# Optimization experiments

Measured on AMD Instinct MI355X. Metric: run time of the kernel, lower is better.

## Reference

```python
import jax, jax.numpy as jnp
import numpy as np

PERIOD = 0.1


def setup_inputs() -> dict:
    key = jax.random.key(0)
    ks = jax.random.split(key, 16)
    B, N, C, P = 2, 3072, 4, 4
    E, H, T, F, L = 512, 8, 256, 64, 4
    Nt = N // P

    def rn(k, shape, scale=0.02):
        return jax.random.normal(k, shape, jnp.float32) * scale

    return {
        "x": jax.random.normal(ks[0], (B, N, C), jnp.float32),
        "t": jax.random.normal(ks[1], (B, T), jnp.float32),
        "vec_map": jax.random.normal(ks[2], (B, N, 3), jnp.float32),
        # RelativeBias dense: freq features -> heads
        "W_rb": rn(ks[3], (F, H)),
        "b_rb": jnp.zeros((H,), jnp.float32),
        # patch embedding dense: P*C -> E
        "W_embed": rn(ks[4], (P * C, E), 0.1),
        "b_embed": jnp.zeros((E,), jnp.float32),
        "pos_emb": rn(ks[5], (Nt, E)),
        # stacked per-block params (leading dim L = n_blocks)
        "ada1_W1": rn(ks[6], (L, T, T)),
        "ada1_b1": jnp.zeros((L, T), jnp.float32),
        "ada1_W2": rn(ks[7], (L, T, 3 * E)),
        "ada1_b2": jnp.zeros((L, 3 * E), jnp.float32),
        "qkv_W": rn(ks[8], (L, E, 3 * E)),
        "qkv_b": jnp.zeros((L, 3 * E), jnp.float32),
        "out_W": rn(ks[9], (L, E, E)),
        "out_b": jnp.zeros((L, E), jnp.float32),
        "ada2_W1": rn(ks[10], (L, T, T)),
        "ada2_b1": jnp.zeros((L, T), jnp.float32),
        "ada2_W2": rn(ks[11], (L, T, 3 * E)),
        "ada2_b2": jnp.zeros((L, 3 * E), jnp.float32),
        "mlp_W1": rn(ks[12], (L, E, 4 * E)),
        "mlp_b1": jnp.zeros((L, 4 * E), jnp.float32),
        "mlp_W2": rn(ks[13], (L, 4 * E, E)),
        "mlp_b2": jnp.zeros((L, E), jnp.float32),
    }


def _layernorm(y):
    # flax LayerNorm(use_bias=False, use_scale=False), eps=1e-6
    mu = jnp.mean(y, axis=-1, keepdims=True)
    var = jnp.mean(jnp.square(y - mu), axis=-1, keepdims=True)
    return (y - mu) * jax.lax.rsqrt(var + 1e-6)


def _adaln(t, W1, b1, W2, b2):
    h = jax.nn.silu(t @ W1 + b1)
    m = (h @ W2 + b2)[..., None, :]  # (B, 1, 3E)
    return jnp.split(m, 3, axis=-1)


def reference(x, t, vec_map, W_rb, b_rb, W_embed, b_embed, pos_emb,
              ada1_W1, ada1_b1, ada1_W2, ada1_b2, qkv_W, qkv_b, out_W, out_b,
              ada2_W1, ada2_b1, ada2_W2, ada2_b2, mlp_W1, mlp_b1, mlp_W2, mlp_b2):
    B, N, C = x.shape
    Nt, E = pos_emb.shape
    P = N // Nt
    F, H = W_rb.shape
    hd = E // H

    # patchify tokens: (B, N, C) -> (B, Nt, P*C); mean vec per patch
    xp = x.reshape(B, Nt, P * C)
    vp = vec_map.reshape(B, Nt, P, 3).mean(axis=-2)

    # relative bias logits (B, Nt, Nt, H)
    v = vp / jnp.linalg.norm(vp, axis=-1, keepdims=True)
    dif = v[..., :, None, :] - v[..., None, :, :]
    dot = 1.0 - 0.5 * jnp.sum(dif * dif, axis=-1)
    angle = jnp.arccos(jnp.clip(dot, -1.0, 1.0)) / 0.005
    freqs = jnp.linspace(0, 1, F // 2) / PERIOD
    ph = freqs * angle[..., None]  # (B, Nt, Nt, F/2)
    pos = jnp.concatenate((jnp.sin(ph), jnp.cos(ph)), axis=-1)
    bias = pos @ W_rb + b_rb

    # patch embed + learned positional embedding
    h0 = xp @ W_embed + b_embed + pos_emb
    inv_sqrt_hd = 1.0 / jnp.sqrt(jnp.float32(hd))

    def block(xc, params):
        (aW1, ab1, aW2, ab2, qW, qb, oW, ob,
         cW1, cb1, cW2, cb2, mW1, mb1, mW2, mb2) = params
        g1, be1, al1 = _adaln(t, aW1, ab1, aW2, ab2)
        y = (g1 + 1.0) * _layernorm(xc) + be1
        qkv = (y @ qW + qb).reshape(B, Nt, H, 3, hd)
        q, k, vv = qkv[..., 0, :], qkv[..., 1, :], qkv[..., 2, :]
        logits = jnp.einsum('bqht,bkht->bqkh', q, k) * inv_sqrt_hd + bias
        logits = logits - jnp.max(logits, axis=-2, keepdims=True)
        attn = jax.nn.softmax(logits, axis=-2)  # softmax over keys (K axis)
        y = jnp.einsum('bqkh,bkht->bqht', attn, vv).reshape(B, Nt, E)
        y = y @ oW + ob
        xc = xc + al1 * y / jnp.sqrt(1.0 + al1 * al1)
        g2, be2, al2 = _adaln(t, cW1, cb1, cW2, cb2)
        y = (g2 + 1.0) * _layernorm(xc) + be2
        y = jax.nn.gelu(y @ mW1 + mb1) @ mW2 + mb2
        xc = xc + al2 * y / jnp.sqrt(1.0 + al2 * al2)
        return xc, None

    params = (ada1_W1, ada1_b1, ada1_W2, ada1_b2, qkv_W, qkv_b, out_W, out_b,
              ada2_W1, ada2_b1, ada2_W2, ada2_b2, mlp_W1, mlp_b1, mlp_W2, mlp_b2)
    out, _ = jax.lax.scan(block, h0, params)
    return out
```

## Files before the change

### kernel.cpp

```cpp
#include <hip/hip_runtime.h>
#include <hip/hip_bf16.h>


#define NT 768
#define EDIM 512
#define E3 1536
#define E4 2048
#define NH 8
#define TB 2

typedef unsigned short ushort_t;
typedef __attribute__((ext_vector_type(8))) short bf16x8;
typedef __attribute__((ext_vector_type(4))) float f32x4;

#define GLOAD(src, dst) __builtin_amdgcn_global_load_lds( \
    (const __attribute__((address_space(1))) unsigned int*)(src), \
    (__attribute__((address_space(3))) unsigned int*)(dst), 16, 0, 0)

__device__ inline float b2f(ushort_t u) {
    unsigned int i = ((unsigned int)u) << 16; float f;
    __builtin_memcpy(&f, &i, 4); return f;
}
__device__ inline ushort_t f2b(float f) {
    __hip_bfloat16 h = __float2bfloat16(f);
    ushort_t u; __builtin_memcpy(&u, &h, 2); return u;
}
__device__ inline float gelu_tanh(float u) {
    float z = 1.5957691216057308f * (u + 0.044715f * u * u * u);
    z = fminf(z, 40.f);
    float t = __expf(z);
    float th = (t - 1.f) / (t + 1.f);
    return 0.5f * u * (1.f + th);
}

__global__ __launch_bounds__(256) void k_bias(const float* __restrict__ vm, const float* __restrict__ W_rb,
                                              const float* __restrict__ b_rb, ushort_t* __restrict__ biasT) {
    int bq = blockIdx.x; int b = bq / NT, q = bq % NT;
    __shared__ float sv[NT * 3];
    int tid = threadIdx.x, lane = tid & 63, wave = tid >> 6;
    for (int i = tid; i < NT; i += 256) {
        const float* vp = vm + ((long)b * 3072 + i * 4) * 3;
        float s0 = vp[0] + vp[3] + vp[6] + vp[9];
        float s1 = vp[1] + vp[4] + vp[7] + vp[10];
        float s2 = vp[2] + vp[5] + vp[8] + vp[11];
        float inv = rsqrtf(s0 * s0 + s1 * s1 + s2 * s2);
        sv[i * 3 + 0] = s0 * inv; sv[i * 3 + 1] = s1 * inv; sv[i * 3 + 2] = s2 * inv;
    }

    int g = lane >> 4, col = lane & 15;
    ushort_t tw[16];
    #pragma unroll
    for (int j = 0; j < 8; ++j) {
        float wsv = (col < 8) ? W_rb[(g * 8 + j) * 8 + col] : 0.f;
        float wcv = (col < 8) ? W_rb[(32 + g * 8 + j) * 8 + col] : 0.f;
        tw[j] = f2b(wsv); tw[8 + j] = f2b(wcv);
    }
    bf16x8 bsf, bcf;
    __builtin_memcpy(&bsf, tw, 16);
    __builtin_memcpy(&bcf, tw + 8, 16);
    float brh = (col < 8) ? b_rb[col] : 0.f;
    __syncthreads();

    float vq0 = sv[q * 3], vq1 = sv[q * 3 + 1], vq2 = sv[q * 3 + 2];
    float gf = (float)(8 * g);

    for (int it = 0; it < 12; ++it) {
        int tile = (it * 4 + wave) * 16;
        int p = tile + col;
        float d0 = vq0 - sv[p * 3], d1 = vq1 - sv[p * 3 + 1], d2 = vq2 - sv[p * 3 + 2];
        float dot = 1.f - 0.5f * (d0 * d0 + d1 * d1 + d2 * d2);
        dot = fminf(1.f, fmaxf(-1.f, dot));
        float theta = acosf(dot) * (2000.f / 31.f);
        float s1, c1; __sincosf(theta, &s1, &c1);
        float sg, cg; __sincosf(theta * gf, &sg, &cg);
        ushort_t fs[16];
        #pragma unroll
        for (int j = 0; j < 8; ++j) {
            fs[j] = f2b(sg); fs[8 + j] = f2b(cg);
            float ns = sg * c1 + cg * s1;
            cg = cg * c1 - sg * s1;
            sg = ns;
        }
        bf16x8 asf, acf;
        __builtin_memcpy(&asf, fs, 16);
        __builtin_memcpy(&acf, fs + 8, 16);
        f32x4 acc = {0.f, 0.f, 0.f, 0.f};
        acc = __builtin_amdgcn_mfma_f32_16x16x32_bf16(asf, bsf, acc, 0, 0, 0);
        acc = __builtin_amdgcn_mfma_f32_16x16x32_bf16(acf, bcf, acc, 0, 0, 0);
        if (col < 8) {
            ushort_t o[4];
            #pragma unroll
            for (int r = 0; r < 4; ++r) o[r] = f2b(acc[r] + brh);
            long off = (long)(b * 8 + col) * NT * NT + (long)q * NT + tile + 4 * g;
            uint2 pk;
            pk.x = (unsigned int)o[0] | ((unsigned int)o[1] << 16);
            pk.y = (unsigned int)o[2] | ((unsigned int)o[3] << 16);
            *(uint2*)(biasT + off) = pk;
        }
    }
}

__global__ __launch_bounds__(256) void k_embed(const float* __restrict__ x, const float* __restrict__ W,
                                               const float* __restrict__ be, const float* __restrict__ pe,
                                               float* __restrict__ xc) {
    int row = blockIdx.x; int nt = row % NT;
    __shared__ float sx[16];
    int tid = threadIdx.x;
    if (tid < 16) sx[tid] = x[row * 16 + tid];
    __syncthreads();
    for (int e = tid; e < EDIM; e += 256) {
        float a = be[e] + pe[nt * EDIM + e];
        #pragma unroll
        for (int j = 0; j < 16; ++j) a += sx[j] * W[j * EDIM + e];
        xc[(long)row * EDIM + e] = a;
    }
}

__global__ __launch_bounds__(256) void k_adaln(const float* __restrict__ t,
    const float* __restrict__ a1W1, const float* __restrict__ a1b1, const float* __restrict__ a1W2, const float* __restrict__ a1b2,
    const float* __restrict__ a2W1, const float* __restrict__ a2b1, const float* __restrict__ a2W2, const float* __restrict__ a2b2,
    float* __restrict__ ada) {
    int blk = blockIdx.x; int b = blk & 1, lw = blk >> 1; int which = lw & 1, l = lw >> 1;
    const float* W1 = (which ? a2W1 : a1W1) + (long)l * 256 * 256;
    const float* b1 = (which ? a2b1 : a1b1) + l * 256;
    const float* W2 = (which ? a2W2 : a1W2) + (long)l * 256 * E3;
    const float* b2 = (which ? a2b2 : a1b2) + l * E3;
    __shared__ float st[256], sh[256];
    int tid = threadIdx.x;
    st[tid] = t[b * 256 + tid];
    __syncthreads();
    float a = b1[tid];
    for (int i = 0; i < 256; ++i) a += st[i] * W1[i * 256 + tid];
    sh[tid] = a / (1.f + __expf(-a));
    __syncthreads();
    int c = blockIdx.y * 256 + tid;
    float m = b2[c];
    for (int i = 0; i < 256; ++i) m += sh[i] * W2[i * E3 + c];
    ada[(long)(lw * 2 + b) * E3 + c] = m;
}

__global__ __launch_bounds__(256) void k_lnmod(const float* __restrict__ xc, const float* __restrict__ ada,
                                               ushort_t* __restrict__ out, int lw) {
    int row = blockIdx.x; int b = row / NT;
    const float* ap = ada + (long)(lw * 2 + b) * E3;
    int tid = threadIdx.x;
    float2 vv = *(const float2*)(xc + (long)row * EDIM + tid * 2);
    float s1 = vv.x + vv.y, s2 = vv.x * vv.x + vv.y * vv.y;
    for (int o = 32; o; o >>= 1) { s1 += __shfl_down(s1, o); s2 += __shfl_down(s2, o); }
    __shared__ float sr[8];
    if ((tid & 63) == 0) { sr[tid >> 6] = s1; sr[4 + (tid >> 6)] = s2; }
    __syncthreads();
    s1 = sr[0] + sr[1] + sr[2] + sr[3];
    s2 = sr[4] + sr[5] + sr[6] + sr[7];
    float mu = s1 * (1.f / 512.f);
    float var = s2 * (1.f / 512.f) - mu * mu;
    float inv = rsqrtf(var + 1e-6f);
    int e = tid * 2;
    float r0 = (ap[e] + 1.f) * ((vv.x - mu) * inv) + ap[512 + e];
    float r1 = (ap[e + 1] + 1.f) * ((vv.y - mu) * inv) + ap[512 + e + 1];
    unsigned int pk = (unsigned int)f2b(r0) | ((unsigned int)f2b(r1) << 16);
    ((unsigned int*)out)[(long)row * 256 + tid] = pk;
}

__global__ __launch_bounds__(256) void k_wTall(
        const float* __restrict__ qkvW, const float* __restrict__ outW,
        const float* __restrict__ m1W, const float* __restrict__ m2W,
        ushort_t* __restrict__ qkvWt, ushort_t* __restrict__ outWt,
        ushort_t* __restrict__ m1Wt, ushort_t* __restrict__ m2Wt) {
    int idx = blockIdx.x, l = blockIdx.y;
    const float* W; ushort_t* Wt; int Kd, Nd, ntile, ktile;
    if (idx < 192)      { W = qkvW; Wt = qkvWt; Kd = 512;  Nd = 1536; ntile = idx % 24; ktile = idx / 24; }
    else if (idx < 256) { W = outW; Wt = outWt; Kd = 512;  Nd = 512;  idx -= 192; ntile = idx % 8;  ktile = idx / 8; }
    else if (idx < 512) { W = m1W;  Wt = m1Wt;  Kd = 512;  Nd = 2048; idx -= 256; ntile = idx % 32; ktile = idx / 32; }
    else                { W = m2W;  Wt = m2Wt;  Kd = 2048; Nd = 512;  idx -= 512; ntile = idx % 8;  ktile = idx / 8; }
    const float* Wp = W + (long)l * Kd * Nd;
    ushort_t* Wtp = Wt + (long)l * Kd * Nd;
    int n0 = ntile * 64, k0 = ktile * 64;
    __shared__ float s[64][65];
    int tid = threadIdx.x;
    #pragma unroll
    for (int it = 0; it < 4; ++it) {
        int i2 = tid + it * 256;
        int r = i2 >> 4, c4 = (i2 & 15) * 4;
        float4 vv = *(const float4*)(Wp + (long)(k0 + r) * Nd + n0 + c4);
        s[r][c4] = vv.x; s[r][c4 + 1] = vv.y; s[r][c4 + 2] = vv.z; s[r][c4 + 3] = vv.w;
    }
    __syncthreads();
    #pragma unroll
    for (int it = 0; it < 4; ++it) {
        int i2 = tid + it * 256;
        int rn = i2 >> 4, ck = (i2 & 15) * 4;
        long base = (long)(n0 + rn) * Kd + k0 + ck;
        #pragma unroll
        for (int j = 0; j < 4; ++j) Wtp[base + j] = f2b(s[ck + j][rn]);
    }
}

__global__ __launch_bounds__(256) void k_attn(const ushort_t* __restrict__ qkv16,
        const ushort_t* __restrict__ vT, const ushort_t* __restrict__ biasT,
        ushort_t* __restrict__ attnb) {
    int qt = blockIdx.x, bh = blockIdx.y;
    int b = bh >> 3, h = bh & 7;
    __shared__ __align__(16) ushort_t Ks[2][4096];
    __shared__ __align__(16) ushort_t Vs[2][4096];
    __shared__ __align__(16) ushort_t Bi[2][4096];
    int tid = threadIdx.x, lane = tid & 63, wave = tid >> 6;
    int g = lane >> 4, c = lane & 15;
    int ls = lane & 7, lr = lane >> 3;
    int stg_col = (ls ^ lr) * 8;
    int q0 = qt * 64;

    bf16x8 aq[2];
    {
        const ushort_t* qp = qkv16 + ((long)(b * NT + q0 + wave * 16 + c) * E3) + h * 192;
        aq[0] = *(const bf16x8*)(qp + g * 8);
        aq[1] = *(const bf16x8*)(qp + 32 + g * 8);
    }
    float m_r[4], l_r[4];
    f32x4 o_acc[4];
    #pragma unroll
    for (int rr = 0; rr < 4; ++rr) { m_r[rr] = -1e30f; l_r[rr] = 0.f; }
    #pragma unroll
    for (int nf = 0; nf < 4; ++nf) o_acc[nf] = f32x4{0.f, 0.f, 0.f, 0.f};

#define STAGEA(buf, kt) { \
        int k0_ = (kt) * 64; \
        _Pragma("unroll") \
        for (int is = 0; is < 2; ++is) { \
            int row = is * 32 + wave * 8 + lr; \
            int dstb = (is * 32 + wave * 8) * 64; \
            GLOAD(qkv16 + (long)(b * NT + k0_ + row) * E3 + h * 192 + 64 + stg_col, &Ks[buf][dstb]); \
            GLOAD(vT + ((long)bh * 64 + row) * NT + k0_ + stg_col, &Vs[buf][dstb]); \
            GLOAD(biasT + (long)bh * NT * NT + (long)(q0 + row) * NT + k0_ + ls * 8, &Bi[buf][dstb]); \
        } }

    STAGEA(0, 0);
    __syncthreads();
    int cur = 0;
    for (int kt = 0; kt < 12; ++kt) {
        if (kt + 1 < 12) STAGEA(cur ^ 1, kt + 1);
        f32x4 s[4];
        #pragma unroll
        for (int nf = 0; nf < 4; ++nf) {
            s[nf] = f32x4{0.f, 0.f, 0.f, 0.f};
            #pragma unroll
            for (int kh = 0; kh < 2; ++kh) {
                int row = nf * 16 + c;
                bf16x8 bk = *(const bf16x8*)(&Ks[cur][row * 64 + (((kh * 4 + g) ^ (row & 7))) * 8]);
                s[nf] = __builtin_amdgcn_mfma_f32_16x16x32_bf16(aq[kh], bk, s[nf], 0, 0, 0);
            }
        }
        float p[4][4], mt[4];
        #pragma unroll
        for (int rr = 0; rr < 4; ++rr) {
            int ql = wave * 16 + g * 4 + rr;
            #pragma unroll
            for (int nf = 0; nf < 4; ++nf)
                p[nf][rr] = s[nf][rr] * 0.125f + b2f(Bi[cur][ql * 64 + nf * 16 + c]);
            float mx = fmaxf(fmaxf(p[0][rr], p[1][rr]), fmaxf(p[2][rr], p[3][rr]));
            mx = fmaxf(mx, __shfl_xor(mx, 1));
            mx = fmaxf(mx, __shfl_xor(mx, 2));
            mx = fmaxf(mx, __shfl_xor(mx, 4));
            mx = fmaxf(mx, __shfl_xor(mx, 8));
            mt[rr] = mx;
        }
        #pragma unroll
        for (int rr = 0; rr < 4; ++rr) {
            float mnew = fmaxf(m_r[rr], mt[rr]);
            float sc = __expf(m_r[rr] - mnew);
            m_r[rr] = mnew;
            float rsum = 0.f;
            #pragma unroll
            for (int nf = 0; nf < 4; ++nf) {
                p[nf][rr] = __expf(p[nf][rr] - mnew);
                rsum += p[nf][rr];
            }
            rsum += __shfl_xor(rsum, 1); rsum += __shfl_xor(rsum, 2);
            rsum += __shfl_xor(rsum, 4); rsum += __shfl_xor(rsum, 8);
            l_r[rr] = l_r[rr] * sc + rsum;
            #pragma unroll
            for (int nf = 0; nf < 4; ++nf) o_acc[nf][rr] *= sc;
        }
        #pragma unroll
        for (int nf = 0; nf < 4; ++nf) {
            int kl = nf * 16 + c;
            int slot = kl >> 3, win = kl & 7;
            #pragma unroll
            for (int rr = 0; rr < 4; ++rr) {
                int ql = wave * 16 + g * 4 + rr;
                Bi[cur][ql * 64 + ((slot ^ (ql & 7)) * 8) + win] = f2b(p[nf][rr]);
            }
        }
        asm volatile("s_waitcnt lgkmcnt(0)" ::: "memory");
        bf16x8 ap[2];
        #pragma unroll
        for (int kh = 0; kh < 2; ++kh) {
            int ql = wave * 16 + c;
            ap[kh] = *(const bf16x8*)(&Bi[cur][ql * 64 + (((kh * 4 + g) ^ (ql & 7))) * 8]);
        }
        #pragma unroll
        for (int nf = 0; nf < 4; ++nf) {
            #pragma unroll
            for (int kh = 0; kh < 2; ++kh) {
                int row = nf * 16 + c;
                bf16x8 bv = *(const bf16x8*)(&Vs[cur][row * 64 + (((kh * 4 + g) ^ (row & 7))) * 8]);
                o_acc[nf] = __builtin_amdgcn_mfma_f32_16x16x32_bf16(ap[kh], bv, o_acc[nf], 0, 0, 0);
            }
        }
        __syncthreads();
        cur ^= 1;
    }
#undef STAGEA
    #pragma unroll
    for (int nf = 0; nf < 4; ++nf) {
        #pragma unroll
        for (int rr = 0; rr < 4; ++rr) {
            int ql = wave * 16 + g * 4 + rr;
            Ks[0][ql * 64 + nf * 16 + c] = f2b(o_acc[nf][rr] / l_r[rr]);
        }
    }
    asm volatile("s_waitcnt lgkmcnt(0)" ::: "memory");
    __syncthreads();
    int orow = wave * 16 + (lane >> 2);
    int ocol = (lane & 3) * 16;
    const ushort_t* srcO = &Ks[0][orow * 64 + ocol];
    ushort_t* dstO = attnb + (long)(b * NT + q0 + orow) * EDIM + h * 64 + ocol;
    *(bf16x8*)(dstO) = *(const bf16x8*)(srcO);
    *(bf16x8*)(dstO + 8) = *(const bf16x8*)(srcO + 8);
}

template<int EPI>
__global__ __launch_bounds__(256) void k_mm64(
        const ushort_t* __restrict__ A0, const ushort_t* __restrict__ B0,
        const float* __restrict__ bias, const float* __restrict__ xin,
        const float* __restrict__ ada, int lw, void* __restrict__ C0,
        int K, int lda, int ldb, int ldc, ushort_t* __restrict__ vTout) {
    __shared__ __align__(16) ushort_t As[2][4096];
    __shared__ __align__(16) ushort_t Bs[2][4096];
    int tid = threadIdx.x, lane = tid & 63, wave = tid >> 6;
    int wm = wave >> 1, wn = wave & 1;
    int m0 = blockIdx.y * 64, n0 = blockIdx.x * 64;
    int lr = lane >> 3, ls = lane & 7;
    int stg_col = (ls ^ lr) * 8;
    int r = lane & 15, g = lane >> 4, rs = r & 7;
    int nt = K >> 6;

    f32x4 acc[2][2];
    #pragma unroll
    for (int i = 0; i < 2; ++i)
        #pragma unroll
        for (int j = 0; j < 2; ++j) acc[i][j] = f32x4{0.f, 0.f, 0.f, 0.f};

#define STAGE64(buf, t) { \
        int k0_ = (t) * 64; \
        _Pragma("unroll") \
        for (int c0 = 0; c0 < 4; ++c0) { \
            int ch = wave * 4 + c0; \
            if (ch < 8) { \
                GLOAD(A0 + (long)(m0 + ch * 8 + lr) * lda + k0_ + stg_col, &As[buf][ch * 512]); \
            } else { \
                GLOAD(B0 + (long)(n0 + (ch - 8) * 8 + lr) * ldb + k0_ + stg_col, &Bs[buf][(ch - 8) * 512]); \
            } \
        } }

    STAGE64(0, 0);
    __syncthreads();
    int cur = 0;
    for (int t = 0; t < nt; ++t) {
        if (t + 1 < nt) STAGE64(cur ^ 1, t + 1);
        bf16x8 af[2][2], bfr[2][2];
        #pragma unroll
        for (int i = 0; i < 2; ++i) {
            int row = wm * 32 + i * 16 + r;
            #pragma unroll
            for (int kh = 0; kh < 2; ++kh)
                af[i][kh] = *(const bf16x8*)(&As[cur][row * 64 + (((kh * 4 + g) ^ rs)) * 8]);
        }
        #pragma unroll
        for (int j = 0; j < 2; ++j) {
            int row = wn * 32 + j * 16 + r;
            #pragma unroll
            for (int kh = 0; kh < 2; ++kh)
                bfr[j][kh] = *(const bf16x8*)(&Bs[cur][row * 64 + (((kh * 4 + g) ^ rs)) * 8]);
        }
        #pragma unroll
        for (int kh = 0; kh < 2; ++kh)
            #pragma unroll
            for (int i = 0; i < 2; ++i)
                #pragma unroll
                for (int j = 0; j < 2; ++j)
                    acc[i][j] = __builtin_amdgcn_mfma_f32_16x16x32_bf16(af[i][kh], bfr[j][kh], acc[i][j], 0, 0, 0);
        __syncthreads();
        cur ^= 1;
    }
#undef STAGE64

    int gr4 = g * 4, cL = lane & 15;
    if constexpr (EPI == 0 || EPI == 1) {
        ushort_t* C = (ushort_t*)C0;
        #pragma unroll
        for (int i = 0; i < 2; ++i) {
            int mrow = m0 + wm * 32 + i * 16 + gr4;
            #pragma unroll
            for (int j = 0; j < 2; ++j) {
                int n = n0 + wn * 32 + j * 16 + cL;
                float bn = bias[n];
                ushort_t o[4];
                #pragma unroll
                for (int rr = 0; rr < 4; ++rr) {
                    float vv = acc[i][j][rr] + bn;
                    if constexpr (EPI == 1) vv = gelu_tanh(vv);
                    o[rr] = f2b(vv);
                    C[(long)(mrow + rr) * ldc + n] = o[rr];
                }
                if constexpr (EPI == 0) {
                    if (vTout) {
                        int seg = n % 192;
                        if (seg >= 128) {
                            int h = n / 192, d = seg - 128;
                            int b2 = (mrow >= NT) ? 1 : 0;
                            int tok = mrow - b2 * NT;
                            uint2 pk;
                            pk.x = (unsigned int)o[0] | ((unsigned int)o[1] << 16);
                            pk.y = (unsigned int)o[2] | ((unsigned int)o[3] << 16);
                            *(uint2*)(vTout + ((long)((b2 * 8 + h) * 64 + d)) * NT + tok) = pk;
                        }
                    }
                }
            }
        }
    } else {
        float* C = (float*)C0;
        #pragma unroll
        for (int i = 0; i < 2; ++i) {
            int mrow = m0 + wm * 32 + i * 16 + gr4;
            int bb = (mrow >= NT) ? 1 : 0;
            const float* al = ada + (long)(lw * 2 + bb) * E3 + 1024;
            #pragma unroll
            for (int j = 0; j < 2; ++j) {
                int n = n0 + wn * 32 + j * 16 + cL;
                float a = al[n];
                float sc = a * rsqrtf(1.f + a * a);
                float bn = bias[n];
                #pragma unroll
                for (int rr = 0; rr < 4; ++rr) {
                    long idx = (long)(mrow + rr) * ldc + n;
                    C[idx] = xin[idx] + sc * (acc[i][j][rr] + bn);
                }
            }
        }
    }
}

extern "C" void kernel_launch(void* const* d_in, const int* in_sizes, int n_in,
                              void* d_out, int out_size, void* d_ws, size_t ws_size,
                              hipStream_t stream) {
    const float* x       = (const float*)d_in[0];
    const float* t       = (const float*)d_in[1];
    const float* vec_map = (const float*)d_in[2];
    const float* W_rb    = (const float*)d_in[3];
    const float* b_rb    = (const float*)d_in[4];
    const float* W_embed = (const float*)d_in[5];
    const float* b_embed = (const float*)d_in[6];
    const float* pos_emb = (const float*)d_in[7];
    const float* a1W1    = (const float*)d_in[8];
    const float* a1b1    = (const float*)d_in[9];
    const float* a1W2    = (const float*)d_in[10];
    const float* a1b2    = (const float*)d_in[11];
    const float* qkv_W   = (const float*)d_in[12];
    const float* qkv_b   = (const float*)d_in[13];
    const float* out_W   = (const float*)d_in[14];
    const float* out_b   = (const float*)d_in[15];
    const float* a2W1    = (const float*)d_in[16];
    const float* a2b1    = (const float*)d_in[17];
    const float* a2W2    = (const float*)d_in[18];
    const float* a2b2    = (const float*)d_in[19];
    const float* mlp_W1  = (const float*)d_in[20];
    const float* mlp_b1  = (const float*)d_in[21];
    const float* mlp_W2  = (const float*)d_in[22];
    const float* mlp_b2  = (const float*)d_in[23];

    float* ws = (float*)d_ws;
    size_t o = 0;
    ushort_t* biasT = (ushort_t*)(ws + o); o += 4718592;
    float* ada      = ws + o; o += 24576;
    float* xc       = ws + o; o += 786432;
    ushort_t* ln16  = (ushort_t*)(ws + o); o += 393216;
    ushort_t* qkv16 = (ushort_t*)(ws + o); o += 1179648;
    ushort_t* vT    = (ushort_t*)(ws + o); o += 393216;
    ushort_t* attnb = (ushort_t*)(ws + o); o += 393216;
    ushort_t* mlph  = (ushort_t*)(ws + o); o += 1572864;
    ushort_t* qkvWt = (ushort_t*)(ws + o); o += 1572864;
    ushort_t* outWt = (ushort_t*)(ws + o); o += 524288;
    ushort_t* mlp1Wt = (ushort_t*)(ws + o); o += 2097152;
    ushort_t* mlp2Wt = (ushort_t*)(ws + o); o += 2097152;

    k_bias<<<TB * NT, 256, 0, stream>>>(vec_map, W_rb, b_rb, biasT);
    k_embed<<<TB * NT, 256, 0, stream>>>(x, W_embed, b_embed, pos_emb, xc);
    k_adaln<<<dim3(16, 6), 256, 0, stream>>>(t, a1W1, a1b1, a1W2, a1b2, a2W1, a2b1, a2W2, a2b2, ada);
    k_wTall<<<dim3(768, 4), 256, 0, stream>>>(qkv_W, out_W, mlp_W1, mlp_W2,
                                              qkvWt, outWt, mlp1Wt, mlp2Wt);

    for (int l = 0; l < 4; ++l) {
        int lw0 = l * 2, lw1 = l * 2 + 1;
        k_lnmod<<<TB * NT, 256, 0, stream>>>(xc, ada, ln16, lw0);
        k_mm64<0><<<dim3(24, 24), 256, 0, stream>>>(
            ln16, qkvWt + (long)l * 786432, qkv_b + l * E3, nullptr, nullptr, 0,
            qkv16, 512, 512, 512, E3, vT);
        k_attn<<<dim3(12, 16), 256, 0, stream>>>(qkv16, vT, biasT, attnb);
        k_mm64<5><<<dim3(8, 24), 256, 0, stream>>>(
            attnb, outWt + (long)l * 262144, out_b + l * EDIM, xc, ada, lw0,
            xc, 512, 512, 512, EDIM, nullptr);
        k_lnmod<<<TB * NT, 256, 0, stream>>>(xc, ada, ln16, lw1);
        k_mm64<1><<<dim3(32, 24), 256, 0, stream>>>(
            ln16, mlp1Wt + (long)l * 1048576, mlp_b1 + l * E4, nullptr, nullptr, 0,
            mlph, 512, 512, 512, E4, nullptr);
        k_mm64<5><<<dim3(8, 24), 256, 0, stream>>>(
            mlph, mlp2Wt + (long)l * 1048576, mlp_b2 + l * EDIM, xc, ada, lw1,
            (l == 3) ? (float*)d_out : xc, 2048, 2048, 2048, EDIM, nullptr);
    }
}
```

Baseline: 395.4 us.

## Split-K the N=512 GEMMs and fuse the partial reduce with residual and LayerNorm

```diff
diff --git a/kernel.cpp b/kernel.cpp
--- a/kernel.cpp
+++ b/kernel.cpp
@@ -100,20 +100,39 @@
     }
 }
 
-__global__ __launch_bounds__(256) void k_embed(const float* __restrict__ x, const float* __restrict__ W,
-                                               const float* __restrict__ be, const float* __restrict__ pe,
-                                               float* __restrict__ xc) {
-    int row = blockIdx.x; int nt = row % NT;
+__global__ __launch_bounds__(256) void k_embedln(const float* __restrict__ x, const float* __restrict__ W,
+                                                 const float* __restrict__ be, const float* __restrict__ pe,
+                                                 const float* __restrict__ ada,
+                                                 float* __restrict__ xc, ushort_t* __restrict__ ln16) {
+    int row = blockIdx.x; int nt = row % NT, b = row / NT;
     __shared__ float sx[16];
-    int tid = threadIdx.x;
+    __shared__ float sm[8];
+    int tid = threadIdx.x, w = tid >> 6;
     if (tid < 16) sx[tid] = x[row * 16 + tid];
     __syncthreads();
-    for (int e = tid; e < EDIM; e += 256) {
-        float a = be[e] + pe[nt * EDIM + e];
-        #pragma unroll
-        for (int j = 0; j < 16; ++j) a += sx[j] * W[j * EDIM + e];
-        xc[(long)row * EDIM + e] = a;
-    }
+    float a0 = be[tid] + pe[nt * EDIM + tid];
+    float a1 = be[tid + 256] + pe[nt * EDIM + tid + 256];
+    #pragma unroll
+    for (int j = 0; j < 16; ++j) {
+        a0 += sx[j] * W[j * EDIM + tid];
+        a1 += sx[j] * W[j * EDIM + tid + 256];
+    }
+    xc[(long)row * EDIM + tid] = a0;
+    xc[(long)row * EDIM + tid + 256] = a1;
+    float s1 = a0 + a1, s2 = a0 * a0 + a1 * a1;
+    for (int o = 32; o; o >>= 1) { s1 += __shfl_down(s1, o); s2 += __shfl_down(s2, o); }
+    if ((tid & 63) == 0) { sm[w] = s1; sm[4 + w] = s2; }
+    __syncthreads();
+    s1 = sm[0] + sm[1] + sm[2] + sm[3];
+    s2 = sm[4] + sm[5] + sm[6] + sm[7];
+    float mu = s1 * (1.f / 512.f);
+    float var = s2 * (1.f / 512.f) - mu * mu;
+    float inv = rsqrtf(var + 1e-6f);
+    const float* ap = ada + (long)b * E3;
+    float r0 = (ap[tid] + 1.f) * ((a0 - mu) * inv) + ap[512 + tid];
+    float r1 = (ap[tid + 256] + 1.f) * ((a1 - mu) * inv) + ap[512 + tid + 256];
+    ln16[(long)row * EDIM + tid] = f2b(r0);
+    ln16[(long)row * EDIM + tid + 256] = f2b(r1);
 }
 
 __global__ __launch_bounds__(256) void k_adaln(const float* __restrict__ t,
@@ -137,29 +156,6 @@
     float m = b2[c];
     for (int i = 0; i < 256; ++i) m += sh[i] * W2[i * E3 + c];
     ada[(long)(lw * 2 + b) * E3 + c] = m;
-}
-
-__global__ __launch_bounds__(256) void k_lnmod(const float* __restrict__ xc, const float* __restrict__ ada,
-                                               ushort_t* __restrict__ out, int lw) {
-    int row = blockIdx.x; int b = row / NT;
-    const float* ap = ada + (long)(lw * 2 + b) * E3;
-    int tid = threadIdx.x;
-    float2 vv = *(const float2*)(xc + (long)row * EDIM + tid * 2);
-    float s1 = vv.x + vv.y, s2 = vv.x * vv.x + vv.y * vv.y;
-    for (int o = 32; o; o >>= 1) { s1 += __shfl_down(s1, o); s2 += __shfl_down(s2, o); }
-    __shared__ float sr[8];
-    if ((tid & 63) == 0) { sr[tid >> 6] = s1; sr[4 + (tid >> 6)] = s2; }
-    __syncthreads();
-    s1 = sr[0] + sr[1] + sr[2] + sr[3];
-    s2 = sr[4] + sr[5] + sr[6] + sr[7];
-    float mu = s1 * (1.f / 512.f);
-    float var = s2 * (1.f / 512.f) - mu * mu;
-    float inv = rsqrtf(var + 1e-6f);
-    int e = tid * 2;
-    float r0 = (ap[e] + 1.f) * ((vv.x - mu) * inv) + ap[512 + e];
-    float r1 = (ap[e + 1] + 1.f) * ((vv.y - mu) * inv) + ap[512 + e + 1];
-    unsigned int pk = (unsigned int)f2b(r0) | ((unsigned int)f2b(r1) << 16);
-    ((unsigned int*)out)[(long)row * 256 + tid] = pk;
 }
 
 __global__ __launch_bounds__(256) void k_wTall(
@@ -240,6 +236,7 @@
     for (int kt = 0; kt < 12; ++kt) {
         if (kt + 1 < 12) STAGEA(cur ^ 1, kt + 1);
         f32x4 s[4];
+        __builtin_amdgcn_s_setprio(1);
         #pragma unroll
         for (int nf = 0; nf < 4; ++nf) {
             s[nf] = f32x4{0.f, 0.f, 0.f, 0.f};
@@ -250,6 +247,7 @@
                 s[nf] = __builtin_amdgcn_mfma_f32_16x16x32_bf16(aq[kh], bk, s[nf], 0, 0, 0);
             }
         }
+        __builtin_amdgcn_s_setprio(0);
         float p[4][4], mt[4];
         #pragma unroll
         for (int rr = 0; rr < 4; ++rr) {
@@ -298,6 +296,7 @@
             int ql = wave * 16 + c;
             ap[kh] = *(const bf16x8*)(&Bi[cur][ql * 64 + (((kh * 4 + g) ^ (ql & 7))) * 8]);
         }
+        __builtin_amdgcn_s_setprio(1);
         #pragma unroll
         for (int nf = 0; nf < 4; ++nf) {
             #pragma unroll
@@ -307,6 +306,7 @@
                 o_acc[nf] = __builtin_amdgcn_mfma_f32_16x16x32_bf16(ap[kh], bv, o_acc[nf], 0, 0, 0);
             }
         }
+        __builtin_amdgcn_s_setprio(0);
         __syncthreads();
         cur ^= 1;
     }
@@ -332,9 +332,8 @@
 template<int EPI>
 __global__ __launch_bounds__(256) void k_mm64(
         const ushort_t* __restrict__ A0, const ushort_t* __restrict__ B0,
-        const float* __restrict__ bias, const float* __restrict__ xin,
-        const float* __restrict__ ada, int lw, void* __restrict__ C0,
-        int K, int lda, int ldb, int ldc, ushort_t* __restrict__ vTout) {
+        const float* __restrict__ bias, void* __restrict__ C0,
+        int Kchunk, int lda, int ldb, int ldc, ushort_t* __restrict__ vTout) {
     __shared__ __align__(16) ushort_t As[2][4096];
     __shared__ __align__(16) ushort_t Bs[2][4096];
     int tid = threadIdx.x, lane = tid & 63, wave = tid >> 6;
@@ -343,7 +342,9 @@
     int lr = lane >> 3, ls = lane & 7;
     int stg_col = (ls ^ lr) * 8;
     int r = lane & 15, g = lane >> 4, rs = r & 7;
-    int nt = K >> 6;
+    int nt = Kchunk >> 6;
+    const ushort_t* A = A0 + (long)blockIdx.z * Kchunk;
+    const ushort_t* B = B0 + (long)blockIdx.z * Kchunk;
 
     f32x4 acc[2][2];
     #pragma unroll
@@ -357,9 +358,9 @@
         for (int c0 = 0; c0 < 4; ++c0) { \
             int ch = wave * 4 + c0; \
             if (ch < 8) { \
-                GLOAD(A0 + (long)(m0 + ch * 8 + lr) * lda + k0_ + stg_col, &As[buf][ch * 512]); \
+                GLOAD(A + (long)(m0 + ch * 8 + lr) * lda + k0_ + stg_col, &As[buf][ch * 512]); \
             } else { \
-                GLOAD(B0 + (long)(n0 + (ch - 8) * 8 + lr) * ldb + k0_ + stg_col, &Bs[buf][(ch - 8) * 512]); \
+                GLOAD(B + (long)(n0 + (ch - 8) * 8 + lr) * ldb + k0_ + stg_col, &Bs[buf][(ch - 8) * 512]); \
             } \
         } }
 
@@ -430,25 +431,73 @@
             }
         }
     } else {
-        float* C = (float*)C0;
+        float* C = (float*)C0 + (long)blockIdx.z * (1536 * 512);
         #pragma unroll
         for (int i = 0; i < 2; ++i) {
             int mrow = m0 + wm * 32 + i * 16 + gr4;
-            int bb = (mrow >= NT) ? 1 : 0;
-            const float* al = ada + (long)(lw * 2 + bb) * E3 + 1024;
             #pragma unroll
             for (int j = 0; j < 2; ++j) {
                 int n = n0 + wn * 32 + j * 16 + cL;
-                float a = al[n];
-                float sc = a * rsqrtf(1.f + a * a);
-                float bn = bias[n];
                 #pragma unroll
-                for (int rr = 0; rr < 4; ++rr) {
-                    long idx = (long)(mrow + rr) * ldc + n;
-                    C[idx] = xin[idx] + sc * (acc[i][j][rr] + bn);
-                }
+                for (int rr = 0; rr < 4; ++rr)
+                    C[(long)(mrow + rr) * ldc + n] = acc[i][j][rr];
             }
         }
+    }
+}
+
+__global__ __launch_bounds__(256) void k_redln(const float* __restrict__ P, int kSplit,
+        const float* __restrict__ bias, const float* __restrict__ ada,
+        int lw_res, int lw_next,
+        const float* __restrict__ xin, float* __restrict__ xout,
+        ushort_t* __restrict__ lnout) {
+    int tid = threadIdx.x;
+    int row = blockIdx.x * 2 + (tid >> 7);
+    int col = (tid & 127) * 4;
+    int b = (row >= NT) ? 1 : 0;
+    long idx = (long)row * EDIM + col;
+    float4 s = *(const float4*)(P + idx);
+    for (int kc = 1; kc < kSplit; ++kc) {
+        float4 p = *(const float4*)(P + (long)kc * (1536 * 512) + idx);
+        s.x += p.x; s.y += p.y; s.z += p.z; s.w += p.w;
+    }
+    float4 bv = *(const float4*)(bias + col);
+    const float* al = ada + (long)(lw_res * 2 + b) * E3 + 1024;
+    float4 av = *(const float4*)(al + col);
+    float4 xv = *(const float4*)(xin + idx);
+    float4 r;
+    r.x = xv.x + av.x * rsqrtf(1.f + av.x * av.x) * (s.x + bv.x);
+    r.y = xv.y + av.y * rsqrtf(1.f + av.y * av.y) * (s.y + bv.y);
+    r.z = xv.z + av.z * rsqrtf(1.f + av.z * av.z) * (s.z + bv.z);
+    r.w = xv.w + av.w * rsqrtf(1.f + av.w * av.w) * (s.w + bv.w);
+    *(float4*)(xout + idx) = r;
+
+    if (lnout) {
+        float s1 = r.x + r.y + r.z + r.w;
+        float s2 = r.x * r.x + r.y * r.y + r.z * r.z + r.w * r.w;
+        for (int o = 32; o; o >>= 1) { s1 += __shfl_xor(s1, o); s2 += __shfl_xor(s2, o); }
+        __shared__ float sm[8];
+        int w = tid >> 6;
+        if ((tid & 63) == 0) { sm[w] = s1; sm[4 + w] = s2; }
+        __syncthreads();
+        int p2 = (tid >> 7) * 2;
+        s1 = sm[p2] + sm[p2 + 1];
+        s2 = sm[4 + p2] + sm[4 + p2 + 1];
+        float mu = s1 * (1.f / 512.f);
+        float var = s2 * (1.f / 512.f) - mu * mu;
+        float inv = rsqrtf(var + 1e-6f);
+        const float* ap = ada + (long)(lw_next * 2 + b) * E3;
+        float4 gv = *(const float4*)(ap + col);
+        float4 bev = *(const float4*)(ap + 512 + col);
+        ushort_t o4[4];
+        o4[0] = f2b((gv.x + 1.f) * ((r.x - mu) * inv) + bev.x);
+        o4[1] = f2b((gv.y + 1.f) * ((r.y - mu) * inv) + bev.y);
+        o4[2] = f2b((gv.z + 1.f) * ((r.z - mu) * inv) + bev.z);
+        o4[3] = f2b((gv.w + 1.f) * ((r.w - mu) * inv) + bev.w);
+        uint2 pk;
+        pk.x = (unsigned int)o4[0] | ((unsigned int)o4[1] << 16);
+        pk.y = (unsigned int)o4[2] | ((unsigned int)o4[3] << 16);
+        *(uint2*)(lnout + idx) = pk;
     }
 }
 
@@ -494,29 +543,31 @@
     ushort_t* outWt = (ushort_t*)(ws + o); o += 524288;
     ushort_t* mlp1Wt = (ushort_t*)(ws + o); o += 2097152;
     ushort_t* mlp2Wt = (ushort_t*)(ws + o); o += 2097152;
-
+    float* P        = ws + o; o += 3145728;
+
+    k_adaln<<<dim3(16, 6), 256, 0, stream>>>(t, a1W1, a1b1, a1W2, a1b2, a2W1, a2b1, a2W2, a2b2, ada);
     k_bias<<<TB * NT, 256, 0, stream>>>(vec_map, W_rb, b_rb, biasT);
-    k_embed<<<TB * NT, 256, 0, stream>>>(x, W_embed, b_embed, pos_emb, xc);
-    k_adaln<<<dim3(16, 6), 256, 0, stream>>>(t, a1W1, a1b1, a1W2, a1b2, a2W1, a2b1, a2W2, a2b2, ada);
+    k_embedln<<<TB * NT, 256, 0, stream>>>(x, W_embed, b_embed, pos_emb, ada, xc, ln16);
     k_wTall<<<dim3(768, 4), 256, 0, stream>>>(qkv_W, out_W, mlp_W1, mlp_W2,
                                               qkvWt, outWt, mlp1Wt, mlp2Wt);
 
     for (int l = 0; l < 4; ++l) {
         int lw0 = l * 2, lw1 = l * 2 + 1;
-        k_lnmod<<<TB * NT, 256, 0, stream>>>(xc, ada, ln16, lw0);
-        k_mm64<0><<<dim3(24, 24), 256, 0, stream>>>(
-            ln16, qkvWt + (long)l * 786432, qkv_b + l * E3, nullptr, nullptr, 0,
+        k_mm64<0><<<dim3(24, 24, 1), 256, 0, stream>>>(
+            ln16, qkvWt + (long)l * 786432, qkv_b + l * E3,
             qkv16, 512, 512, 512, E3, vT);
         k_attn<<<dim3(12, 16), 256, 0, stream>>>(qkv16, vT, biasT, attnb);
-        k_mm64<5><<<dim3(8, 24), 256, 0, stream>>>(
-            attnb, outWt + (long)l * 262144, out_b + l * EDIM, xc, ada, lw0,
-            xc, 512, 512, 512, EDIM, nullptr);
-        k_lnmod<<<TB * NT, 256, 0, stream>>>(xc, ada, ln16, lw1);
-        k_mm64<1><<<dim3(32, 24), 256, 0, stream>>>(
-            ln16, mlp1Wt + (long)l * 1048576, mlp_b1 + l * E4, nullptr, nullptr, 0,
+        k_mm64<4><<<dim3(8, 24, 2), 256, 0, stream>>>(
+            attnb, outWt + (long)l * 262144, nullptr,
+            P, 256, 512, 512, EDIM, nullptr);
+        k_redln<<<768, 256, 0, stream>>>(P, 2, out_b + l * EDIM, ada, lw0, lw1, xc, xc, ln16);
+        k_mm64<1><<<dim3(32, 24, 1), 256, 0, stream>>>(
+            ln16, mlp1Wt + (long)l * 1048576, mlp_b1 + l * E4,
             mlph, 512, 512, 512, E4, nullptr);
-        k_mm64<5><<<dim3(8, 24), 256, 0, stream>>>(
-            mlph, mlp2Wt + (long)l * 1048576, mlp_b2 + l * EDIM, xc, ada, lw1,
-            (l == 3) ? (float*)d_out : xc, 2048, 2048, 2048, EDIM, nullptr);
-    }
-}
+        k_mm64<4><<<dim3(8, 24, 4), 256, 0, stream>>>(
+            mlph, mlp2Wt + (long)l * 1048576, nullptr,
+            P, 512, 2048, 2048, EDIM, nullptr);
+        k_redln<<<768, 256, 0, stream>>>(P, 4, mlp_b2 + l * EDIM, ada, lw1, lw1 + 1,
+            xc, (l == 3) ? (float*)d_out : xc, (l == 3) ? nullptr : ln16);
+    }
+}
```

New measurement: 347.0 us. 12.2% less time.
